# Kernel optimization log

Hardware: AMD Instinct MI355X
Metric: run time of the kernel (lower is better)

## Reference

```python
import jax, jax.numpy as jnp
import numpy as np
import math

D_MODEL = 1024
NUM_HEADS = 16
HEAD_DIM = D_MODEL // NUM_HEADS
ROPE_THETA = 10000.0
MAX_SEQ_LEN = 4096


def setup_inputs() -> dict:
    key = jax.random.key(0)
    ks = jax.random.split(key, 6)
    sigma = math.sqrt(2.0 / (D_MODEL + D_MODEL))
    def w(k):
        # trunc_normal within [-3sigma, 3sigma] ~ approximate with clipped normal
        return jnp.clip(sigma * jax.random.normal(k, (D_MODEL, D_MODEL), dtype=jnp.float32), -3 * sigma, 3 * sigma)
    x = jax.random.normal(ks[0], (2, 2048, D_MODEL), dtype=jnp.float32)
    token_positions = jnp.arange(2048, dtype=jnp.int64 if jax.config.jax_enable_x64 else jnp.int32)
    return {
        "x": x,
        "wq": w(ks[1]),
        "wk": w(ks[2]),
        "wv": w(ks[3]),
        "wo": w(ks[4]),
        "token_positions": token_positions,
    }


def _rope(t, positions):
    # t: (B, H, S, head_dim); positions: (S,)
    half = HEAD_DIM // 2
    inv_freq = 1.0 / (ROPE_THETA ** (jnp.arange(0, HEAD_DIM, 2, dtype=jnp.float32) / HEAD_DIM))  # (half,)
    freqs = positions.astype(jnp.float32)[:, None] * inv_freq[None, :]  # (S, half)
    cos = jnp.cos(freqs)
    sin = jnp.sin(freqs)
    t_even = t[..., ::2]   # (B,H,S,half)
    t_odd = t[..., 1::2]
    rot_even = t_even * cos - t_odd * sin
    rot_odd = t_even * sin + t_odd * cos
    return jnp.stack([rot_even, rot_odd], axis=-1).reshape(t.shape)


def reference(x, wq, wk, wv, wo, token_positions):
    B, S, _ = x.shape
    def split_heads(t):
        return t.reshape(B, S, NUM_HEADS, HEAD_DIM).transpose(0, 2, 1, 3)  # (B,H,S,Dh)
    q = split_heads(jnp.einsum('bsd,ed->bse', x, wq))
    k = split_heads(jnp.einsum('bsd,ed->bse', x, wk))
    v = split_heads(jnp.einsum('bsd,ed->bse', x, wv))
    q = _rope(q, token_positions)
    k = _rope(k, token_positions)
    scores = jnp.einsum('bhqd,bhkd->bhqk', q, k) / math.sqrt(HEAD_DIM)
    causal = jnp.tril(jnp.ones((S, S), dtype=bool))
    scores = jnp.where(causal, scores, -jnp.inf)
    probs = jax.nn.softmax(scores, axis=-1)
    out = jnp.einsum('bhqk,bhkd->bhqd', probs, v)  # (B,H,S,Dh)
    out = out.transpose(0, 2, 1, 3).reshape(B, S, D_MODEL)
    return jnp.einsum('bsd,ed->bse', out, wo)
```

## Files before the change

### kernel.cpp

```cpp
#include <hip/hip_runtime.h>
#include <hip/hip_bf16.h>


#define D_MODEL 1024
#define NHEADS  16
#define HDIM    64
#define SEQ     2048
#define BATCH   2

typedef unsigned short u16;
typedef __bf16 bf16x8_t __attribute__((ext_vector_type(8)));
typedef float  f32x4_t  __attribute__((ext_vector_type(4)));

__device__ __forceinline__ u16 f2bf(float f) {
    union { __hip_bfloat16 h; u16 u; } cv;
    cv.h = __float2bfloat16(f);
    return cv.u;
}

__device__ __forceinline__ unsigned pk2(float x, float y) {
    union { __hip_bfloat162 h; unsigned u; } cv;
    cv.h = __float22bfloat162_rn(make_float2(x, y));
    return cv.u;
}

__device__ __forceinline__ uint4 pack8(float4 a, float4 b) {
    uint4 u;
    u.x = pk2(a.x, a.y);
    u.y = pk2(a.z, a.w);
    u.z = pk2(b.x, b.y);
    u.w = pk2(b.z, b.w);
    return u;
}

__device__ __forceinline__ bf16x8_t frag_ld(const u16* p) {
    union { uint4 u; bf16x8_t v; } t;
    t.u = *(const uint4*)p;
    return t.v;
}

__device__ __forceinline__ void acc8(uint4 u, float* a) {
    a[0] += __uint_as_float(u.x << 16); a[1] += __uint_as_float(u.x & 0xffff0000u);
    a[2] += __uint_as_float(u.y << 16); a[3] += __uint_as_float(u.y & 0xffff0000u);
    a[4] += __uint_as_float(u.z << 16); a[5] += __uint_as_float(u.z & 0xffff0000u);
    a[6] += __uint_as_float(u.w << 16); a[7] += __uint_as_float(u.w & 0xffff0000u);
}

__device__ __forceinline__ void dma16(const u16* g, u16* l) {
    __builtin_amdgcn_global_load_lds(
        (const __attribute__((address_space(1))) void*)g,
        (__attribute__((address_space(3))) void*)l, 16, 0, 0);
}

__global__ __launch_bounds__(256) void conv_bf16_kernel(
    const float* __restrict__ X, const float* __restrict__ Wq,
    const float* __restrict__ Wk, const float* __restrict__ Wv,
    const float* __restrict__ Wo, u16* __restrict__ Xbf, u16* __restrict__ Wbf)
{
    const size_t gid = (size_t)blockIdx.x * 256 + threadIdx.x;
    const float* src;
    u16* dst;
    size_t off;
    if (gid < (1u << 19)) {
        src = X; dst = Xbf; off = gid;
    } else {
        size_t g = gid - (1u << 19);
        const int wsel = (int)(g >> 17);
        g &= (1u << 17) - 1;
        src = (wsel == 0) ? Wq : (wsel == 1) ? Wk : (wsel == 2) ? Wv : Wo;
        dst = Wbf + ((size_t)wsel << 20);
        off = g;
    }
    const float4 a = *(const float4*)(src + off * 8);
    const float4 b = *(const float4*)(src + off * 8 + 4);
    *(uint4*)(dst + off * 8) = pack8(a, b);
}

__global__ __launch_bounds__(256) void qkv_rope_kernel(
    const u16* __restrict__ Xbf, const u16* __restrict__ Wbf,
    const int* __restrict__ pos,
    u16* __restrict__ Qo, u16* __restrict__ Ko, u16* __restrict__ Vt)
{
    __shared__ __align__(16) u16 smem[24576];
    const int tid = threadIdx.x;
    const int m0 = blockIdx.y * 128;
    const int nv = (int)blockIdx.x;
    const int which = nv >> 4;
    const int nbase = (nv & 15) * 64;
    const u16* __restrict__ Wsrc = Wbf + ((size_t)which << 20);

    const int w = tid >> 6, L = tid & 63, quad = L >> 4, colL = L & 15;
    const int mw = (w & 1) * 64, nw = (w >> 1) * 32;

    const int lrow = L >> 3;
    const int lchk = (L & 7) ^ lrow;
    const u16* ag = Xbf + (size_t)(m0 + 32 * w + lrow) * D_MODEL + lchk * 8;
    const u16* bg = Wsrc + (size_t)(nbase + 16 * w + lrow) * D_MODEL + lchk * 8;

    f32x4_t acc[4][2];
    #pragma unroll
    for (int i = 0; i < 4; ++i)
        #pragma unroll
        for (int j = 0; j < 2; ++j) acc[i][j] = (f32x4_t){0.f, 0.f, 0.f, 0.f};

    #define QKV_STAGE(boff, k0)                                                 \
        {                                                                       \
            u16* al = smem + (boff) + (32 * w) * 64;                            \
            u16* bl = smem + (boff) + 8192 + (16 * w) * 64;                     \
            _Pragma("unroll")                                                   \
            for (int j = 0; j < 4; ++j)                                         \
                dma16(ag + (size_t)j * 8 * D_MODEL + (k0), al + j * 512);       \
            _Pragma("unroll")                                                   \
            for (int j = 0; j < 2; ++j)                                         \
                dma16(bg + (size_t)j * 8 * D_MODEL + (k0), bl + j * 512);       \
        }

    QKV_STAGE(0, 0)
    for (int it = 0; it < 16; ++it) {
        const int boff = (it & 1) * 12288;
        if (it < 15) {
            QKV_STAGE(boff ^ 12288, (it + 1) * 64)
            asm volatile("s_waitcnt vmcnt(6)" ::: "memory");
        } else {
            asm volatile("s_waitcnt vmcnt(0)" ::: "memory");
        }
        __builtin_amdgcn_sched_barrier(0);
        __builtin_amdgcn_s_barrier();
        __builtin_amdgcn_sched_barrier(0);

        const u16* a_s = smem + boff;
        const u16* b_s = smem + boff + 8192;
        #pragma unroll
        for (int kb = 0; kb < 2; ++kb) {
            const int ch = ((kb * 4 + quad) ^ (colL & 7)) * 8;
            bf16x8_t af[4], bf[2];
            #pragma unroll
            for (int t = 0; t < 4; ++t)
                af[t] = frag_ld(a_s + (mw + t * 16 + colL) * 64 + ch);
            #pragma unroll
            for (int t = 0; t < 2; ++t)
                bf[t] = frag_ld(b_s + (nw + t * 16 + colL) * 64 + ch);
            #pragma unroll
            for (int mt = 0; mt < 4; ++mt)
                #pragma unroll
                for (int nt = 0; nt < 2; ++nt)
                    acc[mt][nt] = __builtin_amdgcn_mfma_f32_16x16x32_bf16(
                        af[mt], bf[nt], acc[mt][nt], 0, 0, 0);
        }
        __builtin_amdgcn_s_barrier();
    }

    __syncthreads();
    u16 (*Ts)[68]  = (u16(*)[68])smem;
    u16 (*Ts2)[136] = (u16(*)[136])smem;

    const float C0 = 0.14391156831212787f;
    if (which < 2) {
        const float oscale = (which == 0) ? 0.18033688011112042f : 1.0f;
        float invf[2], sgn[2];
        #pragma unroll
        for (int nt = 0; nt < 2; ++nt) {
            const int n = nbase + nw + nt * 16 + colL;
            const int dd = n & 63;
            invf[nt] = __expf(-(float)(dd & 62) * C0);
            sgn[nt] = (dd & 1) ? 1.0f : -1.0f;
        }
        #pragma unroll
        for (int mt = 0; mt < 4; ++mt) {
            #pragma unroll
            for (int r = 0; r < 4; ++r) {
                const int ml = mw + mt * 16 + quad * 4 + r;
                const int ss = (m0 + ml) & 2047;
                const float p = (float)pos[ss];
                #pragma unroll
                for (int nt = 0; nt < 2; ++nt) {
                    const float v = acc[mt][nt][r];
                    const float partner = __shfl_xor(v, 1);
                    float sn, cs;
                    __sincosf(p * invf[nt], &sn, &cs);
                    Ts[ml][nw + nt * 16 + colL] =
                        f2bf((v * cs + sgn[nt] * sn * partner) * oscale);
                }
            }
        }
    } else {
        #pragma unroll
        for (int mt = 0; mt < 4; ++mt)
            #pragma unroll
            for (int nt = 0; nt < 2; ++nt)
                #pragma unroll
                for (int r = 0; r < 4; ++r)
                    Ts2[nw + nt * 16 + colL][mw + mt * 16 + quad * 4 + r] = f2bf(acc[mt][nt][r]);
    }
    __syncthreads();

    const int hh = nbase >> 6;
    if (which < 2) {
        u16* __restrict__ dst = (which == 0) ? Qo : Ko;
        const int rr0 = tid >> 3;
        const int cc8 = (tid & 7) * 8;
        #pragma unroll
        for (int it = 0; it < 4; ++it) {
            const int ml = rr0 + it * 32;
            const int m = m0 + ml, bb = m >> 11, ss = m & 2047;
            *(uint4*)&dst[((size_t)(bb * NHEADS + hh) * SEQ + ss) * HDIM + cc8] =
                *(const uint4*)&Ts[ml][cc8];
        }
    } else {
        const int rr0 = tid >> 4;
        const int cc8 = (tid & 15) * 8;
        const int bb = m0 >> 11, ss0 = (m0 & 2047) + cc8;
        #pragma unroll
        for (int it = 0; it < 4; ++it) {
            const int nl = rr0 + it * 16;
            *(uint4*)&Vt[((size_t)(bb * NHEADS + hh) * HDIM + nl) * SEQ + ss0] =
                *(const uint4*)&Ts2[nl][cc8];
        }
    }
}

__global__ __launch_bounds__(256) void attn_kernel(
    const u16* __restrict__ Q, const u16* __restrict__ K,
    const u16* __restrict__ Vt, u16* __restrict__ Opart, float* __restrict__ Lpart)
{
    __shared__ __align__(16) u16 Ks[64][64];
    __shared__ __align__(16) u16 Vs[64][64];
    __shared__ __align__(16) u16 Ps[4][16][64];

    const int tid = threadIdx.x;
    const int slot = 79 - (int)blockIdx.x;
    const int g = (slot >= 48) ? 3 : (slot >= 24) ? 2 : (slot >= 8) ? 1 : 0;
    const int t0 = slot - 4 * g * (g + 1);
    const int rr = t0 / (g + 1);
    const int s  = t0 - rr * (g + 1);
    const int qt = 8 * g + rr;

    const int hh = blockIdx.y, bb = blockIdx.z;
    const size_t bh = ((size_t)bb * NHEADS + hh) * (SEQ * HDIM);
    const int q0 = qt * 64;
    const int kt0 = s * 8;
    const int ktend = min(kt0 + 8, qt + 1);
    const size_t gslot = ((size_t)(bb * NHEADS + hh) * 80 + slot);

    const int w = tid >> 6, L = tid & 63, quad = L >> 4, colL = L & 15;
    const int srow = tid >> 2, sc = (tid & 3) * 16;
    const int c7 = colL & 7;
    const int sch0 = (((tid & 3) * 2) ^ (srow & 7)) * 8;
    const int sch1 = (((tid & 3) * 2 + 1) ^ (srow & 7)) * 8;

    const u16* qp = Q + bh + (size_t)(q0 + w * 16 + colL) * HDIM + quad * 8;
    const bf16x8_t aq0 = frag_ld(qp);
    const bf16x8_t aq1 = frag_ld(qp + 32);

    float lsum = 0.f;
    f32x4_t O[4];
    #pragma unroll
    for (int dt = 0; dt < 4; ++dt) O[dt] = (f32x4_t){0.f, 0.f, 0.f, 0.f};

    const u16* kp = K + bh + (size_t)(kt0 * 64 + srow) * HDIM + sc;
    const u16* vp = Vt + bh + (size_t)srow * SEQ + kt0 * 64 + sc;
    uint4 kv0 = *(const uint4*)kp;
    uint4 kv1 = *(const uint4*)(kp + 8);
    uint4 vv0 = *(const uint4*)vp;
    uint4 vv1 = *(const uint4*)(vp + 8);

    for (int kt = kt0; kt < ktend; ++kt) {
        __builtin_amdgcn_s_barrier();
        asm volatile("s_waitcnt vmcnt(0)" ::: "memory");
        __builtin_amdgcn_sched_barrier(0);
        *(uint4*)&Ks[srow][sch0] = kv0;
        *(uint4*)&Ks[srow][sch1] = kv1;
        *(uint4*)&Vs[srow][sch0] = vv0;
        *(uint4*)&Vs[srow][sch1] = vv1;
        if (kt + 1 < ktend) {
            const int k1 = (kt + 1) * 64;
            const u16* kpn = K + bh + (size_t)(k1 + srow) * HDIM + sc;
            kv0 = *(const uint4*)kpn;
            kv1 = *(const uint4*)(kpn + 8);
            const u16* vpn = Vt + bh + (size_t)srow * SEQ + k1 + sc;
            vv0 = *(const uint4*)vpn;
            vv1 = *(const uint4*)(vpn + 8);
        }
        asm volatile("s_waitcnt lgkmcnt(0)" ::: "memory");
        __builtin_amdgcn_sched_barrier(0);
        __builtin_amdgcn_s_barrier();

        const bool diag = (kt == qt);
        const int ntmax = diag ? w : 3;
        const int kbmax = diag ? (w >> 1) : 1;

        f32x4_t S[4];
        #pragma unroll
        for (int nt = 0; nt < 4; ++nt) S[nt] = (f32x4_t){0.f, 0.f, 0.f, 0.f};
        #pragma unroll
        for (int nt = 0; nt < 4; ++nt) {
            if (nt <= ntmax) {
                S[nt] = __builtin_amdgcn_mfma_f32_16x16x32_bf16(
                    frag_ld(&Ks[nt * 16 + colL][(quad ^ c7) * 8]), aq0, S[nt], 0, 0, 0);
                S[nt] = __builtin_amdgcn_mfma_f32_16x16x32_bf16(
                    frag_ld(&Ks[nt * 16 + colL][((quad ^ 4) ^ c7) * 8]), aq1, S[nt], 0, 0, 0);
            }
        }

        if (!diag) {
            #pragma unroll
            for (int nt = 0; nt < 4; ++nt) {
                const float p0 = __builtin_amdgcn_exp2f(S[nt][0]);
                const float p1 = __builtin_amdgcn_exp2f(S[nt][1]);
                const float p2 = __builtin_amdgcn_exp2f(S[nt][2]);
                const float p3 = __builtin_amdgcn_exp2f(S[nt][3]);
                lsum += (p0 + p1) + (p2 + p3);
                uint2 pw;
                pw.x = pk2(p0, p1);
                pw.y = pk2(p2, p3);
                *(uint2*)&Ps[w][colL][((2 * nt + (quad >> 1)) ^ c7) * 8 + (quad & 1) * 4] = pw;
            }
        } else {
            const int qrel = w * 16 + colL;
            #pragma unroll
            for (int nt = 0; nt < 4; ++nt) {
                float p0 = 0.f, p1 = 0.f, p2 = 0.f, p3 = 0.f;
                if (nt <= ntmax) {
                    const int krel = nt * 16 + quad * 4;
                    p0 = (krel + 0 <= qrel) ? __builtin_amdgcn_exp2f(S[nt][0]) : 0.f;
                    p1 = (krel + 1 <= qrel) ? __builtin_amdgcn_exp2f(S[nt][1]) : 0.f;
                    p2 = (krel + 2 <= qrel) ? __builtin_amdgcn_exp2f(S[nt][2]) : 0.f;
                    p3 = (krel + 3 <= qrel) ? __builtin_amdgcn_exp2f(S[nt][3]) : 0.f;
                }
                lsum += (p0 + p1) + (p2 + p3);
                uint2 pw;
                pw.x = pk2(p0, p1);
                pw.y = pk2(p2, p3);
                *(uint2*)&Ps[w][colL][((2 * nt + (quad >> 1)) ^ c7) * 8 + (quad & 1) * 4] = pw;
            }
        }

        asm volatile("s_waitcnt lgkmcnt(0)" ::: "memory");
        __builtin_amdgcn_sched_barrier(0);

        #pragma unroll
        for (int kb = 0; kb < 2; ++kb) {
            if (kb <= kbmax) {
                const int ch = ((kb * 4 + quad) ^ c7) * 8;
                const bf16x8_t ap = frag_ld(&Ps[w][colL][ch]);
                #pragma unroll
                for (int dt = 0; dt < 4; ++dt) {
                    const bf16x8_t bv = frag_ld(&Vs[dt * 16 + colL][ch]);
                    O[dt] = __builtin_amdgcn_mfma_f32_16x16x32_bf16(ap, bv, O[dt], 0, 0, 0);
                }
            }
        }
    }

    {
        float sm = lsum;
        sm += __shfl_xor(sm, 16);
        sm += __shfl_xor(sm, 32);
        if (quad == 0)
            Lpart[gslot * 64 + 16 * w + colL] = sm;
    }

    #pragma unroll
    for (int dt = 0; dt < 4; ++dt)
        #pragma unroll
        for (int r = 0; r < 4; ++r) {
            const int row = quad * 4 + r;
            const int ch = ((2 * dt + (colL >> 3)) ^ (row & 7)) * 8 + (colL & 7);
            Ps[w][row][ch] = f2bf(O[dt][r]);
        }
    asm volatile("s_waitcnt lgkmcnt(0)" ::: "memory");
    __builtin_amdgcn_sched_barrier(0);
    #pragma unroll
    for (int p = 0; p < 2; ++p) {
        const int rowl = (L >> 3) + 8 * p;
        const int ch = ((L & 7) ^ (rowl & 7)) * 8;
        *(uint4*)&Opart[gslot * 4096 + (size_t)(16 * w + rowl) * 64 + (L & 7) * 8] =
            *(const uint4*)&Ps[w][rowl][ch];
    }
}

__global__ __launch_bounds__(256) void combine_kernel(
    const u16* __restrict__ Opart, const float* __restrict__ Lpart,
    u16* __restrict__ AO)
{
    const int qt = blockIdx.x, hh = blockIdx.y, bb = blockIdx.z;
    const int g = qt >> 3;
    const int nsplit = g + 1;
    const int base = 4 * g * (g + 1) + (qt & 7) * (g + 1);
    const int t = threadIdx.x;
    const int q = t >> 2, dg = (t & 3) * 16;
    const size_t slot0 = (size_t)(bb * NHEADS + hh) * 80 + base;

    float acc[16];
    #pragma unroll
    for (int i = 0; i < 16; ++i) acc[i] = 0.f;
    float l = 0.f;
    for (int s = 0; s < nsplit; ++s) {
        const size_t gs = slot0 + s;
        l += Lpart[gs * 64 + q];
        const u16* op = Opart + gs * 4096 + (size_t)q * 64 + dg;
        acc8(*(const uint4*)op, acc);
        acc8(*(const uint4*)(op + 8), acc + 8);
    }
    const float inv = 1.0f / l;
    uint4 o0, o1;
    o0.x = pk2(acc[0] * inv, acc[1] * inv);  o0.y = pk2(acc[2] * inv, acc[3] * inv);
    o0.z = pk2(acc[4] * inv, acc[5] * inv);  o0.w = pk2(acc[6] * inv, acc[7] * inv);
    o1.x = pk2(acc[8] * inv, acc[9] * inv);  o1.y = pk2(acc[10] * inv, acc[11] * inv);
    o1.z = pk2(acc[12] * inv, acc[13] * inv); o1.w = pk2(acc[14] * inv, acc[15] * inv);
    u16* dst = AO + ((size_t)bb * SEQ + qt * 64 + q) * D_MODEL + hh * HDIM + dg;
    *(uint4*)dst = o0;
    *(uint4*)(dst + 8) = o1;
}

__global__ __launch_bounds__(256) void out_proj_kernel(
    const u16* __restrict__ A, const u16* __restrict__ Wob, float* __restrict__ Out)
{
    __shared__ __align__(16) u16 smem[24576];

    const int tid = threadIdx.x;
    const int m0 = blockIdx.y * 64;
    const int n0 = blockIdx.x * 128;

    const int w = tid >> 6, L = tid & 63, quad = L >> 4, colL = L & 15;
    const int mw = (w & 1) * 32, nw = (w >> 1) * 64;

    const int lrow = L >> 3;
    const int lchk = (L & 7) ^ lrow;

    f32x4_t acc[2][4];
    #pragma unroll
    for (int i = 0; i < 2; ++i)
        #pragma unroll
        for (int j = 0; j < 4; ++j) acc[i][j] = (f32x4_t){0.f, 0.f, 0.f, 0.f};

    #define OP_STAGE(boff, k0)                                                  \
        {                                                                       \
            _Pragma("unroll")                                                   \
            for (int j = 0; j < 6; ++j) {                                       \
                const int R0 = 48 * w + 8 * j;                                  \
                const u16* src = (R0 < 64)                                      \
                    ? A + (size_t)(m0 + R0 + lrow) * D_MODEL + lchk * 8         \
                    : Wob + (size_t)(n0 + R0 - 64 + lrow) * D_MODEL + lchk * 8; \
                dma16(src + (k0), smem + (boff) + R0 * 64);                     \
            }                                                                   \
        }

    OP_STAGE(0, 0)
    for (int it = 0; it < 16; ++it) {
        const int boff = (it & 1) * 12288;
        if (it < 15) {
            OP_STAGE(boff ^ 12288, (it + 1) * 64)
            asm volatile("s_waitcnt vmcnt(6)" ::: "memory");
        } else {
            asm volatile("s_waitcnt vmcnt(0)" ::: "memory");
        }
        __builtin_amdgcn_sched_barrier(0);
        __builtin_amdgcn_s_barrier();
        __builtin_amdgcn_sched_barrier(0);

        const u16* a_s = smem + boff;
        const u16* b_s = smem + boff + 4096;
        #pragma unroll
        for (int kb = 0; kb < 2; ++kb) {
            const int ch = ((kb * 4 + quad) ^ (colL & 7)) * 8;
            bf16x8_t af[2], bf[4];
            #pragma unroll
            for (int t = 0; t < 2; ++t)
                af[t] = frag_ld(a_s + (mw + t * 16 + colL) * 64 + ch);
            #pragma unroll
            for (int t = 0; t < 4; ++t)
                bf[t] = frag_ld(b_s + (nw + t * 16 + colL) * 64 + ch);
            #pragma unroll
            for (int mt = 0; mt < 2; ++mt)
                #pragma unroll
                for (int nt = 0; nt < 4; ++nt)
                    acc[mt][nt] = __builtin_amdgcn_mfma_f32_16x16x32_bf16(
                        af[mt], bf[nt], acc[mt][nt], 0, 0, 0);
        }
        __builtin_amdgcn_s_barrier();
    }

    #pragma unroll
    for (int mt = 0; mt < 2; ++mt)
        #pragma unroll
        for (int nt = 0; nt < 4; ++nt)
            #pragma unroll
            for (int r = 0; r < 4; ++r) {
                const int m = m0 + mw + mt * 16 + quad * 4 + r;
                const int n = n0 + nw + nt * 16 + colL;
                Out[(size_t)m * D_MODEL + n] = acc[mt][nt][r];
            }
}

extern "C" void kernel_launch(void* const* d_in, const int* in_sizes, int n_in,
                              void* d_out, int out_size, void* d_ws, size_t ws_size,
                              hipStream_t stream) {
    const float* x  = (const float*)d_in[0];
    const float* wq = (const float*)d_in[1];
    const float* wk = (const float*)d_in[2];
    const float* wv = (const float*)d_in[3];
    const float* wo = (const float*)d_in[4];
    const int* pos  = (const int*)d_in[5];
    float* out = (float*)d_out;

    const size_t NELEM = (size_t)BATCH * NHEADS * SEQ * HDIM;
    u16* Qw  = (u16*)d_ws;
    u16* Kw  = Qw + NELEM;
    u16* Vtw = Kw + NELEM;
    u16* AOw = Vtw + NELEM;
    u16* Xbf = AOw;
    u16* Wbf = AOw + NELEM;
    u16* Opart = Wbf + NELEM;
    float* Lpart = (float*)(Opart + (size_t)2560 * 4096);

    conv_bf16_kernel<<<4096, 256, 0, stream>>>(x, wq, wk, wv, wo, Xbf, Wbf);
    qkv_rope_kernel<<<dim3(48, 32), 256, 0, stream>>>(Xbf, Wbf, pos, Qw, Kw, Vtw);
    attn_kernel<<<dim3(80, NHEADS, BATCH), 256, 0, stream>>>(Qw, Kw, Vtw, Opart, Lpart);
    combine_kernel<<<dim3(32, NHEADS, BATCH), 256, 0, stream>>>(Opart, Lpart, AOw);
    out_proj_kernel<<<dim3(8, 64), 256, 0, stream>>>(AOw, Wbf + 3 * (1u << 20), out);
}
```

Before: 183.9 us.

## Double-buffer attention K/V tiles with direct global-to-LDS DMA loads

The attention kernel now keeps two LDS buffers each for K and V. It fills them with direct global-to-LDS 16-byte loads (dma16) instead of loading into registers and then storing to LDS. The next tile is prefetched into the other buffer while the current one is computed, and a partial vmcnt wait lets the next tile's loads stay in flight. This removes the register staging and the serialized LDS store phase, at the cost of doubling LDS use for K/V, which may lower occupancy.

```diff
diff --git a/kernel.cpp b/kernel.cpp
--- a/kernel.cpp
+++ b/kernel.cpp
@@ -223,8 +223,8 @@
     const u16* __restrict__ Q, const u16* __restrict__ K,
     const u16* __restrict__ Vt, u16* __restrict__ Opart, float* __restrict__ Lpart)
 {
-    __shared__ __align__(16) u16 Ks[64][64];
-    __shared__ __align__(16) u16 Vs[64][64];
+    __shared__ __align__(16) u16 Ks[2][64][64];
+    __shared__ __align__(16) u16 Vs[2][64][64];
     __shared__ __align__(16) u16 Ps[4][16][64];
 
     const int tid = threadIdx.x;
@@ -243,47 +243,46 @@
     const size_t gslot = ((size_t)(bb * NHEADS + hh) * 80 + slot);
 
     const int w = tid >> 6, L = tid & 63, quad = L >> 4, colL = L & 15;
-    const int srow = tid >> 2, sc = (tid & 3) * 16;
     const int c7 = colL & 7;
-    const int sch0 = (((tid & 3) * 2) ^ (srow & 7)) * 8;
-    const int sch1 = (((tid & 3) * 2 + 1) ^ (srow & 7)) * 8;
+    const int lr = L >> 3;
+    const int cs = ((L & 7) ^ lr) * 8;
 
     const u16* qp = Q + bh + (size_t)(q0 + w * 16 + colL) * HDIM + quad * 8;
     const bf16x8_t aq0 = frag_ld(qp);
     const bf16x8_t aq1 = frag_ld(qp + 32);
 
+    const u16* kg = K + bh + (size_t)(16 * w + lr) * HDIM + cs;
+    const u16* vg = Vt + bh + (size_t)(16 * w + lr) * SEQ + cs;
+
+    #define ATTN_STAGE(buf, ktile)                                             \
+        {                                                                      \
+            const size_t ko = (size_t)(ktile) * (64 * HDIM);                   \
+            const size_t vo = (size_t)(ktile) * 64;                            \
+            dma16(kg + ko,            &Ks[buf][16 * w][0]);                    \
+            dma16(kg + ko + 8 * HDIM, &Ks[buf][16 * w + 8][0]);                \
+            dma16(vg + vo,            &Vs[buf][16 * w][0]);                    \
+            dma16(vg + vo + 8 * SEQ,  &Vs[buf][16 * w + 8][0]);                \
+        }
+
     float lsum = 0.f;
     f32x4_t O[4];
     #pragma unroll
     for (int dt = 0; dt < 4; ++dt) O[dt] = (f32x4_t){0.f, 0.f, 0.f, 0.f};
 
-    const u16* kp = K + bh + (size_t)(kt0 * 64 + srow) * HDIM + sc;
-    const u16* vp = Vt + bh + (size_t)srow * SEQ + kt0 * 64 + sc;
-    uint4 kv0 = *(const uint4*)kp;
-    uint4 kv1 = *(const uint4*)(kp + 8);
-    uint4 vv0 = *(const uint4*)vp;
-    uint4 vv1 = *(const uint4*)(vp + 8);
+    ATTN_STAGE(0, kt0)
 
     for (int kt = kt0; kt < ktend; ++kt) {
+        const int buf = kt & 1;
         __builtin_amdgcn_s_barrier();
-        asm volatile("s_waitcnt vmcnt(0)" ::: "memory");
-        __builtin_amdgcn_sched_barrier(0);
-        *(uint4*)&Ks[srow][sch0] = kv0;
-        *(uint4*)&Ks[srow][sch1] = kv1;
-        *(uint4*)&Vs[srow][sch0] = vv0;
-        *(uint4*)&Vs[srow][sch1] = vv1;
         if (kt + 1 < ktend) {
-            const int k1 = (kt + 1) * 64;
-            const u16* kpn = K + bh + (size_t)(k1 + srow) * HDIM + sc;
-            kv0 = *(const uint4*)kpn;
-            kv1 = *(const uint4*)(kpn + 8);
-            const u16* vpn = Vt + bh + (size_t)srow * SEQ + k1 + sc;
-            vv0 = *(const uint4*)vpn;
-            vv1 = *(const uint4*)(vpn + 8);
-        }
-        asm volatile("s_waitcnt lgkmcnt(0)" ::: "memory");
+            ATTN_STAGE(buf ^ 1, kt + 1)
+            asm volatile("s_waitcnt vmcnt(4)" ::: "memory");
+        } else {
+            asm volatile("s_waitcnt vmcnt(0)" ::: "memory");
+        }
         __builtin_amdgcn_sched_barrier(0);
         __builtin_amdgcn_s_barrier();
+        __builtin_amdgcn_sched_barrier(0);
 
         const bool diag = (kt == qt);
         const int ntmax = diag ? w : 3;
@@ -296,9 +295,9 @@
         for (int nt = 0; nt < 4; ++nt) {
             if (nt <= ntmax) {
                 S[nt] = __builtin_amdgcn_mfma_f32_16x16x32_bf16(
-                    frag_ld(&Ks[nt * 16 + colL][(quad ^ c7) * 8]), aq0, S[nt], 0, 0, 0);
+                    frag_ld(&Ks[buf][nt * 16 + colL][(quad ^ c7) * 8]), aq0, S[nt], 0, 0, 0);
                 S[nt] = __builtin_amdgcn_mfma_f32_16x16x32_bf16(
-                    frag_ld(&Ks[nt * 16 + colL][((quad ^ 4) ^ c7) * 8]), aq1, S[nt], 0, 0, 0);
+                    frag_ld(&Ks[buf][nt * 16 + colL][((quad ^ 4) ^ c7) * 8]), aq1, S[nt], 0, 0, 0);
             }
         }
 
@@ -345,7 +344,7 @@
                 const bf16x8_t ap = frag_ld(&Ps[w][colL][ch]);
                 #pragma unroll
                 for (int dt = 0; dt < 4; ++dt) {
-                    const bf16x8_t bv = frag_ld(&Vs[dt * 16 + colL][ch]);
+                    const bf16x8_t bv = frag_ld(&Vs[buf][dt * 16 + colL][ch]);
                     O[dt] = __builtin_amdgcn_mfma_f32_16x16x32_bf16(ap, bv, O[dt], 0, 0, 0);
                 }
             }
```

Result: faster. 180.2 us (-2.0%).

## Drop split-KV attention and combine kernel; normalize output inside attention

Applied to the files above, without the earlier changes.

Attention now runs one block per query tile over the full causal key range and divides by the row sum in-kernel before writing bf16 output directly. This removes the partial-output buffers and the separate combine launch and its memory traffic. In exchange, parallelism drops and per-block work becomes highly unbalanced, with the longest tiles looping over all key tiles. A head-dependent rotation of tile index is used to spread long and short tiles.

```diff
diff --git a/kernel.cpp b/kernel.cpp
--- a/kernel.cpp
+++ b/kernel.cpp
@@ -37,13 +37,6 @@
     union { uint4 u; bf16x8_t v; } t;
     t.u = *(const uint4*)p;
     return t.v;
-}
-
-__device__ __forceinline__ void acc8(uint4 u, float* a) {
-    a[0] += __uint_as_float(u.x << 16); a[1] += __uint_as_float(u.x & 0xffff0000u);
-    a[2] += __uint_as_float(u.y << 16); a[3] += __uint_as_float(u.y & 0xffff0000u);
-    a[4] += __uint_as_float(u.z << 16); a[5] += __uint_as_float(u.z & 0xffff0000u);
-    a[6] += __uint_as_float(u.w << 16); a[7] += __uint_as_float(u.w & 0xffff0000u);
 }
 
 __device__ __forceinline__ void dma16(const u16* g, u16* l) {
@@ -221,26 +214,20 @@
 
 __global__ __launch_bounds__(256) void attn_kernel(
     const u16* __restrict__ Q, const u16* __restrict__ K,
-    const u16* __restrict__ Vt, u16* __restrict__ Opart, float* __restrict__ Lpart)
+    const u16* __restrict__ Vt, u16* __restrict__ AO)
 {
     __shared__ __align__(16) u16 Ks[64][64];
     __shared__ __align__(16) u16 Vs[64][64];
     __shared__ __align__(16) u16 Ps[4][16][64];
+    __shared__ __align__(16) float Linv[4][16];
 
     const int tid = threadIdx.x;
-    const int slot = 79 - (int)blockIdx.x;
-    const int g = (slot >= 48) ? 3 : (slot >= 24) ? 2 : (slot >= 8) ? 1 : 0;
-    const int t0 = slot - 4 * g * (g + 1);
-    const int rr = t0 / (g + 1);
-    const int s  = t0 - rr * (g + 1);
-    const int qt = 8 * g + rr;
-
     const int hh = blockIdx.y, bb = blockIdx.z;
+    const int qt = ((int)blockIdx.x + hh) & 31;
+    const int ktend = qt + 1;
+
     const size_t bh = ((size_t)bb * NHEADS + hh) * (SEQ * HDIM);
     const int q0 = qt * 64;
-    const int kt0 = s * 8;
-    const int ktend = min(kt0 + 8, qt + 1);
-    const size_t gslot = ((size_t)(bb * NHEADS + hh) * 80 + slot);
 
     const int w = tid >> 6, L = tid & 63, quad = L >> 4, colL = L & 15;
     const int srow = tid >> 2, sc = (tid & 3) * 16;
@@ -257,14 +244,14 @@
     #pragma unroll
     for (int dt = 0; dt < 4; ++dt) O[dt] = (f32x4_t){0.f, 0.f, 0.f, 0.f};
 
-    const u16* kp = K + bh + (size_t)(kt0 * 64 + srow) * HDIM + sc;
-    const u16* vp = Vt + bh + (size_t)srow * SEQ + kt0 * 64 + sc;
+    const u16* kp = K + bh + (size_t)srow * HDIM + sc;
+    const u16* vp = Vt + bh + (size_t)srow * SEQ + sc;
     uint4 kv0 = *(const uint4*)kp;
     uint4 kv1 = *(const uint4*)(kp + 8);
     uint4 vv0 = *(const uint4*)vp;
     uint4 vv1 = *(const uint4*)(vp + 8);
 
-    for (int kt = kt0; kt < ktend; ++kt) {
+    for (int kt = 0; kt < ktend; ++kt) {
         __builtin_amdgcn_s_barrier();
         asm volatile("s_waitcnt vmcnt(0)" ::: "memory");
         __builtin_amdgcn_sched_barrier(0);
@@ -352,13 +339,17 @@
         }
     }
 
-    {
-        float sm = lsum;
-        sm += __shfl_xor(sm, 16);
-        sm += __shfl_xor(sm, 32);
-        if (quad == 0)
-            Lpart[gslot * 64 + 16 * w + colL] = sm;
-    }
+    float sm = lsum;
+    sm += __shfl_xor(sm, 16);
+    sm += __shfl_xor(sm, 32);
+    if (quad == 0)
+        Linv[w][colL] = 1.0f / sm;
+    asm volatile("s_waitcnt lgkmcnt(0)" ::: "memory");
+    __builtin_amdgcn_sched_barrier(0);
+    float inv[4];
+    #pragma unroll
+    for (int r = 0; r < 4; ++r)
+        inv[r] = Linv[w][quad * 4 + r];
 
     #pragma unroll
     for (int dt = 0; dt < 4; ++dt)
@@ -366,7 +357,7 @@
         for (int r = 0; r < 4; ++r) {
             const int row = quad * 4 + r;
             const int ch = ((2 * dt + (colL >> 3)) ^ (row & 7)) * 8 + (colL & 7);
-            Ps[w][row][ch] = f2bf(O[dt][r]);
+            Ps[w][row][ch] = f2bf(O[dt][r] * inv[r]);
         }
     asm volatile("s_waitcnt lgkmcnt(0)" ::: "memory");
     __builtin_amdgcn_sched_barrier(0);
@@ -374,43 +365,10 @@
     for (int p = 0; p < 2; ++p) {
         const int rowl = (L >> 3) + 8 * p;
         const int ch = ((L & 7) ^ (rowl & 7)) * 8;
-        *(uint4*)&Opart[gslot * 4096 + (size_t)(16 * w + rowl) * 64 + (L & 7) * 8] =
-            *(const uint4*)&Ps[w][rowl][ch];
-    }
-}
-
-__global__ __launch_bounds__(256) void combine_kernel(
-    const u16* __restrict__ Opart, const float* __restrict__ Lpart,
-    u16* __restrict__ AO)
-{
-    const int qt = blockIdx.x, hh = blockIdx.y, bb = blockIdx.z;
-    const int g = qt >> 3;
-    const int nsplit = g + 1;
-    const int base = 4 * g * (g + 1) + (qt & 7) * (g + 1);
-    const int t = threadIdx.x;
-    const int q = t >> 2, dg = (t & 3) * 16;
-    const size_t slot0 = (size_t)(bb * NHEADS + hh) * 80 + base;
-
-    float acc[16];
-    #pragma unroll
-    for (int i = 0; i < 16; ++i) acc[i] = 0.f;
-    float l = 0.f;
-    for (int s = 0; s < nsplit; ++s) {
-        const size_t gs = slot0 + s;
-        l += Lpart[gs * 64 + q];
-        const u16* op = Opart + gs * 4096 + (size_t)q * 64 + dg;
-        acc8(*(const uint4*)op, acc);
-        acc8(*(const uint4*)(op + 8), acc + 8);
-    }
-    const float inv = 1.0f / l;
-    uint4 o0, o1;
-    o0.x = pk2(acc[0] * inv, acc[1] * inv);  o0.y = pk2(acc[2] * inv, acc[3] * inv);
-    o0.z = pk2(acc[4] * inv, acc[5] * inv);  o0.w = pk2(acc[6] * inv, acc[7] * inv);
-    o1.x = pk2(acc[8] * inv, acc[9] * inv);  o1.y = pk2(acc[10] * inv, acc[11] * inv);
-    o1.z = pk2(acc[12] * inv, acc[13] * inv); o1.w = pk2(acc[14] * inv, acc[15] * inv);
-    u16* dst = AO + ((size_t)bb * SEQ + qt * 64 + q) * D_MODEL + hh * HDIM + dg;
-    *(uint4*)dst = o0;
-    *(uint4*)(dst + 8) = o1;
+        u16* dst = AO + ((size_t)bb * SEQ + q0 + 16 * w + rowl) * D_MODEL
+                      + hh * HDIM + (L & 7) * 8;
+        *(uint4*)dst = *(const uint4*)&Ps[w][rowl][ch];
+    }
 }
 
 __global__ __launch_bounds__(256) void out_proj_kernel(
@@ -511,12 +469,9 @@
     u16* AOw = Vtw + NELEM;
     u16* Xbf = AOw;
     u16* Wbf = AOw + NELEM;
-    u16* Opart = Wbf + NELEM;
-    float* Lpart = (float*)(Opart + (size_t)2560 * 4096);
 
     conv_bf16_kernel<<<4096, 256, 0, stream>>>(x, wq, wk, wv, wo, Xbf, Wbf);
     qkv_rope_kernel<<<dim3(48, 32), 256, 0, stream>>>(Xbf, Wbf, pos, Qw, Kw, Vtw);
-    attn_kernel<<<dim3(80, NHEADS, BATCH), 256, 0, stream>>>(Qw, Kw, Vtw, Opart, Lpart);
-    combine_kernel<<<dim3(32, NHEADS, BATCH), 256, 0, stream>>>(Opart, Lpart, AOw);
+    attn_kernel<<<dim3(32, NHEADS, BATCH), 256, 0, stream>>>(Qw, Kw, Vtw, AOw);
     out_proj_kernel<<<dim3(8, 64), 256, 0, stream>>>(AOw, Wbf + 3 * (1u << 20), out);
 }
```

After: 188.8 us. 1.03x slower.
